# Kernel tuning notes

Measured on AMD Instinct MI355X. Metric: run time of the kernel, lower is better.

Reference implementation:

```python
import jax, jax.numpy as jnp
import numpy as np

B, N = 8192, 128
ALPHA, BETA = 0.5, 0.5
SIGMA1 = 0.01  # prior diagonal variance used in the temporal KL term


def setup_inputs() -> dict:
    key = jax.random.key(0)
    k1, k2, k3, k4, k5 = jax.random.split(key, 5)
    y = jax.random.normal(k1, (B, N), dtype=jnp.float32)
    mu = jax.random.normal(k2, (B, N), dtype=jnp.float32)
    lmbda = jax.random.uniform(k3, (B, N), dtype=jnp.float32, minval=0.5, maxval=2.0)
    psi = 0.1 * jax.random.normal(k4, (B, N, N), dtype=jnp.float32)
    # nu must be > n + 1 so the NIW variance is positive
    nu = jax.random.uniform(k5, (B, N), dtype=jnp.float32, minval=N + 2.0, maxval=N + 12.0)
    return {"y": y, "mu": mu, "lmbda": lmbda, "psi": psi, "nu": nu}


def reference(y, mu, lmbda, psi, nu):
    n = mu.shape[-1]
    y = jnp.nan_to_num(y, nan=0.0)

    # niw_var = diagonal(exp(psi) / (lmbda*(nu-n-1))[...,None]); only the
    # diagonal of psi contributes, so extract it first (same math, less traffic).
    psi_diag = jnp.diagonal(psi, axis1=-2, axis2=-1)              # [B, n]
    niw_var = jnp.exp(psi_diag) / (lmbda * (nu - n - 1.0))        # [B, n]

    # Multivariate KL between diag-Gaussians N(y, SIGMA1*I) and N(mu, diag(niw_var)),
    # with diagonal det/inverse/trace reduced to elementwise ops.
    mu_diff = mu - y
    term_1 = jnp.sum(jnp.log(niw_var), axis=-1) - n * jnp.log(jnp.asarray(SIGMA1, niw_var.dtype))
    term_2 = jnp.sum(SIGMA1 / niw_var, axis=-1)
    term_3 = jnp.sum(mu_diff * mu_diff / niw_var, axis=-1)
    kl = 0.5 * (term_1 - n + term_2 + term_3)                     # [B]
    temporal = jnp.sum(kl)                                        # 'sum' reduction -> scalar

    # L1 evidential error term
    evidence = lmbda + nu                                         # [B, n]
    error = jnp.mean(jnp.sum(jnp.abs(y - mu) * evidence, axis=-1))

    loss = ALPHA * temporal + BETA * error
    return loss, temporal, error
```

## Files before the change

kernel.cpp:

```cpp
#include <hip/hip_runtime.h>
#include <math.h>

#define BB 8192
#define NN 128

typedef float vf4 __attribute__((ext_vector_type(4)));

constexpr int BLOCK = 256;
constexpr int EPT = 4;
constexpr int GRID = (BB * NN) / (BLOCK * EPT);

__global__ __launch_bounds__(BLOCK) void niw_reduce_kernel(
    const float* __restrict__ y, const float* __restrict__ mu,
    const float* __restrict__ lmbda, const float* __restrict__ psi,
    const float* __restrict__ nu, float* __restrict__ partials)
{
    const int t = blockIdx.x * BLOCK + threadIdx.x;
    const int e = t * EPT;
    const int b = e >> 7;
    const int j = e & 127;

    const float* prow = psi + (size_t)b * (NN * NN) + (size_t)j * (NN + 1);
    const float pd[4] = {prow[0], prow[129], prow[258], prow[387]};

    const vf4 yv  = *reinterpret_cast<const vf4*>(y + e);
    const vf4 muv = *reinterpret_cast<const vf4*>(mu + e);
    const vf4 lmv = *reinterpret_cast<const vf4*>(lmbda + e);
    const vf4 nuv = *reinterpret_cast<const vf4*>(nu + e);

    float s1 = 0.f, s2 = 0.f, s3 = 0.f, s4 = 0.f;
#pragma unroll
    for (int k = 0; k < 4; ++k) {
        float yk = yv[k];
        yk = (yk != yk) ? 0.0f : yk;
        const float d = muv[k] - yk;
        const float denom = lmv[k] * (nuv[k] - (float)(NN + 1));
        s1 += pd[k] - __logf(denom);
        const float inv_v = denom * __expf(-pd[k]);
        s2 += inv_v;
        s3 += d * d * inv_v;
        s4 += fabsf(d) * (lmv[k] + nuv[k]);
    }

#pragma unroll
    for (int off = 32; off > 0; off >>= 1) {
        s1 += __shfl_down(s1, off);
        s2 += __shfl_down(s2, off);
        s3 += __shfl_down(s3, off);
        s4 += __shfl_down(s4, off);
    }

    __shared__ float sh[4][4];
    const int wave = threadIdx.x >> 6;
    const int lane = threadIdx.x & 63;
    if (lane == 0) {
        sh[wave][0] = s1; sh[wave][1] = s2; sh[wave][2] = s3; sh[wave][3] = s4;
    }
    __syncthreads();
    if (threadIdx.x == 0) {
        vf4 p;
        p[0] = sh[0][0] + sh[1][0] + sh[2][0] + sh[3][0];
        p[1] = sh[0][1] + sh[1][1] + sh[2][1] + sh[3][1];
        p[2] = sh[0][2] + sh[1][2] + sh[2][2] + sh[3][2];
        p[3] = sh[0][3] + sh[1][3] + sh[2][3] + sh[3][3];
        *reinterpret_cast<vf4*>(partials + (size_t)blockIdx.x * 4) = p;
    }
}

__global__ __launch_bounds__(256) void niw_finalize_kernel(
    const float* __restrict__ partials, float* __restrict__ out)
{
    double t1 = 0, t2 = 0, t3 = 0, t4 = 0;
    for (int i = threadIdx.x; i < GRID; i += 256) {
        const vf4 p = *reinterpret_cast<const vf4*>(partials + (size_t)i * 4);
        t1 += p[0]; t2 += p[1]; t3 += p[2]; t4 += p[3];
    }
#pragma unroll
    for (int off = 32; off > 0; off >>= 1) {
        t1 += __shfl_down(t1, off);
        t2 += __shfl_down(t2, off);
        t3 += __shfl_down(t3, off);
        t4 += __shfl_down(t4, off);
    }
    __shared__ double sh[4][4];
    const int wave = threadIdx.x >> 6;
    const int lane = threadIdx.x & 63;
    if (lane == 0) {
        sh[wave][0] = t1; sh[wave][1] = t2; sh[wave][2] = t3; sh[wave][3] = t4;
    }
    __syncthreads();
    if (threadIdx.x == 0) {
        double S1 = 0, S2 = 0, S3 = 0, S4 = 0;
        for (int w = 0; w < 4; ++w) {
            S1 += sh[w][0]; S2 += sh[w][1]; S3 += sh[w][2]; S4 += sh[w][3];
        }
        const double SIGMA1 = 0.01;
        const double n = (double)NN;
        const double Bd = (double)BB;
        const double temporal =
            0.5 * (S1 - Bd * n * log(SIGMA1) - Bd * n + SIGMA1 * S2 + S3);
        const double error = S4 / Bd;
        const double loss = 0.5 * temporal + 0.5 * error;
        out[0] = (float)loss;
        out[1] = (float)temporal;
        out[2] = (float)error;
    }
}

extern "C" void kernel_launch(void* const* d_in, const int* in_sizes, int n_in,
                              void* d_out, int out_size, void* d_ws, size_t ws_size,
                              hipStream_t stream) {
    const float* y     = (const float*)d_in[0];
    const float* mu    = (const float*)d_in[1];
    const float* lmbda = (const float*)d_in[2];
    const float* psi   = (const float*)d_in[3];
    const float* nu    = (const float*)d_in[4];
    float* out = (float*)d_out;
    float* partials = (float*)d_ws;

    niw_reduce_kernel<<<GRID, BLOCK, 0, stream>>>(y, mu, lmbda, psi, nu, partials);
    niw_finalize_kernel<<<1, 256, 0, stream>>>(partials, out);
}
```

Before: 30.57 us.

## Fuse finalize into reduce kernel via double atomics and last-block counter

Replaces the separate single-block finalize kernel with per-block double-precision atomic adds into workspace accumulators, plus a completion counter so the last block computes the final loss. The workspace is zeroed with a memset before launch. This removes the second kernel launch and its serial tail, at the cost of a memset operation, 1024 contended fp64 atomics on four addresses, and a nondeterministic summation order.

```diff
diff --git a/kernel.cpp b/kernel.cpp
--- a/kernel.cpp
+++ b/kernel.cpp
@@ -10,11 +10,18 @@
 constexpr int EPT = 4;
 constexpr int GRID = (BB * NN) / (BLOCK * EPT);
 
-__global__ __launch_bounds__(BLOCK) void niw_reduce_kernel(
+__global__ __launch_bounds__(BLOCK) void niw_fused_kernel(
     const float* __restrict__ y, const float* __restrict__ mu,
     const float* __restrict__ lmbda, const float* __restrict__ psi,
-    const float* __restrict__ nu, float* __restrict__ partials)
+    const float* __restrict__ nu, char* __restrict__ ws,
+    float* __restrict__ out)
 {
+    unsigned* counter = reinterpret_cast<unsigned*>(ws);
+    double* a1 = reinterpret_cast<double*>(ws + 64);
+    double* a2 = reinterpret_cast<double*>(ws + 192);
+    double* a3 = reinterpret_cast<double*>(ws + 320);
+    double* a4 = reinterpret_cast<double*>(ws + 448);
+
     const int t = blockIdx.x * BLOCK + threadIdx.x;
     const int e = t * EPT;
     const int b = e >> 7;
@@ -57,54 +64,36 @@
         sh[wave][0] = s1; sh[wave][1] = s2; sh[wave][2] = s3; sh[wave][3] = s4;
     }
     __syncthreads();
-    if (threadIdx.x == 0) {
-        vf4 p;
-        p[0] = sh[0][0] + sh[1][0] + sh[2][0] + sh[3][0];
-        p[1] = sh[0][1] + sh[1][1] + sh[2][1] + sh[3][1];
-        p[2] = sh[0][2] + sh[1][2] + sh[2][2] + sh[3][2];
-        p[3] = sh[0][3] + sh[1][3] + sh[2][3] + sh[3][3];
-        *reinterpret_cast<vf4*>(partials + (size_t)blockIdx.x * 4) = p;
-    }
-}
+    if (threadIdx.x != 0) return;
 
-__global__ __launch_bounds__(256) void niw_finalize_kernel(
-    const float* __restrict__ partials, float* __restrict__ out)
-{
-    double t1 = 0, t2 = 0, t3 = 0, t4 = 0;
-    for (int i = threadIdx.x; i < GRID; i += 256) {
-        const vf4 p = *reinterpret_cast<const vf4*>(partials + (size_t)i * 4);
-        t1 += p[0]; t2 += p[1]; t3 += p[2]; t4 += p[3];
-    }
-#pragma unroll
-    for (int off = 32; off > 0; off >>= 1) {
-        t1 += __shfl_down(t1, off);
-        t2 += __shfl_down(t2, off);
-        t3 += __shfl_down(t3, off);
-        t4 += __shfl_down(t4, off);
-    }
-    __shared__ double sh[4][4];
-    const int wave = threadIdx.x >> 6;
-    const int lane = threadIdx.x & 63;
-    if (lane == 0) {
-        sh[wave][0] = t1; sh[wave][1] = t2; sh[wave][2] = t3; sh[wave][3] = t4;
-    }
-    __syncthreads();
-    if (threadIdx.x == 0) {
-        double S1 = 0, S2 = 0, S3 = 0, S4 = 0;
-        for (int w = 0; w < 4; ++w) {
-            S1 += sh[w][0]; S2 += sh[w][1]; S3 += sh[w][2]; S4 += sh[w][3];
-        }
-        const double SIGMA1 = 0.01;
-        const double n = (double)NN;
-        const double Bd = (double)BB;
-        const double temporal =
-            0.5 * (S1 - Bd * n * log(SIGMA1) - Bd * n + SIGMA1 * S2 + S3);
-        const double error = S4 / Bd;
-        const double loss = 0.5 * temporal + 0.5 * error;
-        out[0] = (float)loss;
-        out[1] = (float)temporal;
-        out[2] = (float)error;
-    }
+    const double t1 = (double)sh[0][0] + sh[1][0] + sh[2][0] + sh[3][0];
+    const double t2 = (double)sh[0][1] + sh[1][1] + sh[2][1] + sh[3][1];
+    const double t3 = (double)sh[0][2] + sh[1][2] + sh[2][2] + sh[3][2];
+    const double t4 = (double)sh[0][3] + sh[1][3] + sh[2][3] + sh[3][3];
+
+    atomicAdd(a1, t1);
+    atomicAdd(a2, t2);
+    atomicAdd(a3, t3);
+    atomicAdd(a4, t4);
+    asm volatile("s_waitcnt vmcnt(0)" ::: "memory");
+    const unsigned prev = atomicAdd(counter, 1u);
+    if (prev != (unsigned)(GRID - 1)) return;
+
+    const double S1 = atomicAdd(a1, 0.0);
+    const double S2 = atomicAdd(a2, 0.0);
+    const double S3 = atomicAdd(a3, 0.0);
+    const double S4 = atomicAdd(a4, 0.0);
+
+    const double SIGMA1 = 0.01;
+    const double n = (double)NN;
+    const double Bd = (double)BB;
+    const double temporal =
+        0.5 * (S1 - Bd * n * log(SIGMA1) - Bd * n + SIGMA1 * S2 + S3);
+    const double error = S4 / Bd;
+    const double loss = 0.5 * temporal + 0.5 * error;
+    out[0] = (float)loss;
+    out[1] = (float)temporal;
+    out[2] = (float)error;
 }
 
 extern "C" void kernel_launch(void* const* d_in, const int* in_sizes, int n_in,
@@ -116,8 +105,8 @@
     const float* psi   = (const float*)d_in[3];
     const float* nu    = (const float*)d_in[4];
     float* out = (float*)d_out;
-    float* partials = (float*)d_ws;
 
-    niw_reduce_kernel<<<GRID, BLOCK, 0, stream>>>(y, mu, lmbda, psi, nu, partials);
-    niw_finalize_kernel<<<1, 256, 0, stream>>>(partials, out);
+    hipMemsetAsync(d_ws, 0, 512, stream);
+    niw_fused_kernel<<<GRID, BLOCK, 0, stream>>>(y, mu, lmbda, psi, nu,
+                                                 (char*)d_ws, out);
 }
```

New measurement: 42.45 us. +38.9%, slower.
